# Performance work log

Measured on AMD Instinct MI355X. Metric: run time of the kernel, lower is better.

Reference implementation:

```python
import jax, jax.numpy as jnp
import numpy as np

B, L, D_MODEL, D_K, HEADS, C = 4, 4096, 512, 64, 8, 2
TOPK = int(C * np.log(L))  # int(c * log(input_seq_len)) = 16


def setup_inputs() -> dict:
    key = jax.random.key(0)
    ks = jax.random.split(key, 5)
    q_in = jax.random.normal(ks[0], (B, L, D_MODEL), jnp.float32)
    k_in = jax.random.normal(ks[1], (B, L, D_MODEL), jnp.float32)
    v_in = jax.random.normal(ks[2], (B, L, D_MODEL), jnp.float32)
    Wq = jax.random.normal(ks[3], (D_MODEL, D_K), jnp.float32) / np.sqrt(D_MODEL)
    bq = jax.random.normal(ks[4], (D_K,), jnp.float32) * 0.01
    return {"q_in": q_in, "k_in": k_in, "v_in": v_in, "Wq": Wq, "bq": bq}


def _to_heads(x, Wq, bq):
    # Faithful to original: ALL of q/k/v use the `query` Dense layer, and all
    # heads are identical copies (same projection stacked `heads` times).
    p = x @ Wq + bq                       # [B, L, d_k]
    p = jnp.swapaxes(p, 1, 2)             # [B, d_k, L]  (transpose [0,3,2,1] of [B,L,d,H])
    return jnp.broadcast_to(p[:, None], (p.shape[0], HEADS, D_K, p.shape[-1]))  # [B,H,d,L]


def reference(q_in, k_in, v_in, Wq, bq):
    Q = jnp.fft.fft(_to_heads(q_in, Wq, bq).astype(jnp.complex64), axis=-1)
    K = jnp.fft.fft(_to_heads(k_in, Wq, bq).astype(jnp.complex64), axis=-1)
    V = _to_heads(v_in, Wq, bq)           # [B,H,d,L] float32
    QK = jnp.fft.ifft(Q * jnp.conj(K), axis=-1)   # circular cross-correlation
    qk_abs = jnp.abs(QK)                  # [B,H,d,L]

    vals, idx = jax.lax.top_k(qk_abs, TOPK)       # [B,H,d,k]
    w = jax.nn.softmax(vals, axis=-1)             # softmax over the k lags

    # tf.roll(v, shift=-lag): out[t] = v[(t + lag) mod L]  -> vectorized gather
    t = jnp.arange(L, dtype=jnp.int32)
    gidx = (idx[..., None] + t) % L               # [B,H,d,k,L]
    Vk = jnp.broadcast_to(V[:, :, :, None, :], gidx.shape)
    rolled = jnp.take_along_axis(Vk, gidx, axis=-1)           # [B,H,d,k,L]
    agg = jnp.sum(rolled * w[..., None], axis=3)              # [B,H,d,L]

    out = agg.reshape(agg.shape[0], HEADS * D_K, L)           # [B, H*d, L]
    return jnp.transpose(out, (0, 2, 1))                      # [B, L, H*d]
```

## Files before the change

kernel.cpp:

```cpp
#include <hip/hip_runtime.h>
#include <hip/hip_bf16.h>

#define BQ 4
#define LQ 4096
#define DM 512
#define DK 64
#define NROWS (BQ * DK)
#define TOPK 16
#define CAND 32

typedef __attribute__((ext_vector_type(8))) short short8v;
typedef __attribute__((ext_vector_type(16))) float f32x16;

__device__ __forceinline__ unsigned short f2bf(float x) {
  unsigned u = __builtin_bit_cast(unsigned, x);
  return (unsigned short)((u + 0x7FFFu + ((u >> 16) & 1u)) >> 16);
}
__device__ __forceinline__ float bf2f(unsigned short h) {
  unsigned u = ((unsigned)h) << 16;
  return __builtin_bit_cast(float, u);
}

__device__ __forceinline__ void mfma_drain() {
  __builtin_amdgcn_sched_barrier(0);
  asm volatile("s_nop 7\n\ts_nop 7\n\ts_nop 7\n\ts_nop 7" ::: "memory");
  __builtin_amdgcn_sched_barrier(0);
}

__global__ __launch_bounds__(256) void wprep_kernel(
    const float* __restrict__ Wq, short* __restrict__ wpack) {
  const int ks = blockIdx.x;
  const int t = threadIdx.x;
  const int lane = t & 63, half = t >> 6;
  const int plane = half >> 1, nt = half & 1;
  const int r = nt * 32 + (lane & 31);
  const int kb = 16 * ks + 8 * (lane >> 5);
  short8v o;
#pragma unroll
  for (int i = 0; i < 8; ++i) {
    float v = Wq[(size_t)(kb + i) * DK + r];
    unsigned short h = f2bf(v);
    o[i] = plane ? (short)f2bf(v - bf2f(h)) : (short)h;
  }
  *(short8v*)(&wpack[(((size_t)plane * 2 + nt) * 32 + ks) * 512 + lane * 8]) = o;
}

__global__ __launch_bounds__(256) void proj_kernel(
    const float* __restrict__ q_in, const float* __restrict__ k_in,
    const float* __restrict__ v_in, const short* __restrict__ wpack,
    const float* __restrict__ bq, float* __restrict__ ws) {
  const float* x = blockIdx.z == 0 ? q_in : (blockIdx.z == 1 ? k_in : v_in);
  float* outp = ws + (size_t)blockIdx.z * (size_t)(NROWS * LQ);

  __shared__ __align__(16) float ts[8 * 1088];

  const int tid = threadIdx.x;
  const int l = tid & 63, wv = tid >> 6;
  const int gw = blockIdx.x * 4 + wv;
  const int R0 = gw * 32;
  const int koff = 8 * (l >> 5);

  const float* xb = x + (size_t)(R0 + (l & 31)) * DM + koff;
  const short* wp0 = wpack + l * 8;

  f32x16 acc[2];
#pragma unroll
  for (int nt = 0; nt < 2; ++nt)
#pragma unroll
    for (int i = 0; i < 16; ++i) acc[nt][i] = 0.f;

  float4 a0[8], a1[8];
#pragma unroll
  for (int s = 0; s < 4; ++s) {
    a0[2 * s]     = *(const float4*)(xb + s * 16);
    a0[2 * s + 1] = *(const float4*)(xb + s * 16 + 4);
  }

  short8v wc[4], wn[4];
#define WLOAD(dst, ksg)                                                      \
  do {                                                                       \
    dst[0] = *(const short8v*)(wp0 + (((ksg) + 0) << 9));                    \
    dst[1] = *(const short8v*)(wp0 + (((ksg) + 64) << 9));                   \
    dst[2] = *(const short8v*)(wp0 + (((ksg) + 32) << 9));                   \
    dst[3] = *(const short8v*)(wp0 + (((ksg) + 96) << 9));                   \
  } while (0)
  WLOAD(wc, 0);

#pragma unroll
  for (int kb = 0; kb < 8; ++kb) {
    if (kb < 7) {
#pragma unroll
      for (int s = 0; s < 4; ++s) {
        a1[2 * s]     = *(const float4*)(xb + (kb + 1) * 64 + s * 16);
        a1[2 * s + 1] = *(const float4*)(xb + (kb + 1) * 64 + s * 16 + 4);
      }
    }
#pragma unroll
    for (int s = 0; s < 4; ++s) {
      const int ksg = kb * 4 + s;
      if (ksg < 31) WLOAD(wn, ksg + 1);
      float f[8] = {a0[2 * s].x, a0[2 * s].y, a0[2 * s].z, a0[2 * s].w,
                    a0[2 * s + 1].x, a0[2 * s + 1].y, a0[2 * s + 1].z,
                    a0[2 * s + 1].w};
      short8v ah, al;
#pragma unroll
      for (int i = 0; i < 8; ++i) {
        unsigned short h = f2bf(f[i]);
        ah[i] = (short)h;
        al[i] = (short)f2bf(f[i] - bf2f(h));
      }
      asm volatile(
          "s_nop 4\n\t"
          "v_mfma_f32_32x32x16_bf16 %0, %2, %4, %0\n\t"
          "v_mfma_f32_32x32x16_bf16 %0, %2, %5, %0\n\t"
          "v_mfma_f32_32x32x16_bf16 %0, %3, %4, %0\n\t"
          "v_mfma_f32_32x32x16_bf16 %1, %2, %6, %1\n\t"
          "v_mfma_f32_32x32x16_bf16 %1, %2, %7, %1\n\t"
          "v_mfma_f32_32x32x16_bf16 %1, %3, %6, %1\n\t"
          "s_nop 7\n\t"
          "s_nop 3"
          : "+v"(acc[0]), "+v"(acc[1])
          : "v"(ah), "v"(al), "v"(wc[0]), "v"(wc[1]), "v"(wc[2]), "v"(wc[3]));
      if (ksg < 31) {
#pragma unroll
        for (int i = 0; i < 4; ++i) wc[i] = wn[i];
      }
    }
    if (kb < 7) {
#pragma unroll
      for (int i = 0; i < 8; ++i) a0[i] = a1[i];
    }
  }
#undef WLOAD

  mfma_drain();
  const int b = R0 >> 12, i0 = R0 & (LQ - 1);
  float bb[2] = {bq[l & 31], bq[32 + (l & 31)]};
#pragma unroll
  for (int nt = 0; nt < 2; ++nt) {
    float* area = ts + (wv * 2 + nt) * 1088;
#pragma unroll
    for (int r = 0; r < 16; ++r) {
      int io = (r & 3) + 8 * (r >> 2) + 4 * (l >> 5);
      area[(l & 31) * 34 + io] = acc[nt][r] + bb[nt];
    }
  }
  __syncthreads();
  const int e = l & 15, jg = l >> 4;
#pragma unroll
  for (int nt = 0; nt < 2; ++nt) {
    const float* area = ts + (wv * 2 + nt) * 1088;
#pragma unroll
    for (int p = 0; p < 8; ++p) {
      int jj = jg * 8 + p;
      float2 v = *reinterpret_cast<const float2*>(area + jj * 34 + e * 2);
      *reinterpret_cast<float2*>(
          &outp[((size_t)b * DK + nt * 32 + jj) * LQ + i0 + e * 2]) = v;
    }
  }
}

__global__ __launch_bounds__(512) void corr_topk_kernel(
    const float* __restrict__ qp, const float* __restrict__ kp,
    float* __restrict__ lw) {
  const int row = blockIdx.x;
  const int tid = threadIdx.x;
  __shared__ __align__(16) short qs[3 * 4112 + 4096];
  __shared__ __align__(16) short ks[4096];
  __shared__ __align__(16) float qf[LQ];
  __shared__ __align__(16) float kf[LQ];
  __shared__ unsigned wk[128];
  __shared__ unsigned scand[CAND];
  __shared__ float rS[CAND];
  __shared__ float ordv[TOPK]; __shared__ int ordl[TOPK];

  const float* qr = qp + ((size_t)row << 12);
  const float* kr = kp + ((size_t)row << 12);

  {
    const float4* q4 = (const float4*)qr;
    float4 v0 = q4[tid * 2], v1 = q4[tid * 2 + 1];
    float4 v2 = q4[(tid * 2 + 2) & 1023];
    ((float4*)qf)[tid * 2] = v0;
    ((float4*)qf)[tid * 2 + 1] = v1;
    float f[12] = {v0.x, v0.y, v0.z, v0.w, v1.x, v1.y, v1.z, v1.w,
                   v2.x, v2.y, v2.z, v2.w};
#pragma unroll
    for (int r = 0; r < 4; ++r) {
      short8v o;
#pragma unroll
      for (int i = 0; i < 8; ++i) o[i] = (short)f2bf(f[i + r]);
      *(short8v*)(&qs[r * 4112 + tid * 8]) = o;
    }
    const float4* k4 = (const float4*)kr;
    float4 w0 = k4[tid * 2], w1 = k4[tid * 2 + 1];
    ((float4*)kf)[tid * 2] = w0;
    ((float4*)kf)[tid * 2 + 1] = w1;
    float g[8] = {w0.x, w0.y, w0.z, w0.w, w1.x, w1.y, w1.z, w1.w};
    int Q = tid;
    int Qs = Q ^ ((Q >> 3) & 7);
    short8v o;
#pragma unroll
    for (int i = 0; i < 8; ++i) o[i] = (short)f2bf(g[i]);
    *(short8v*)(&ks[Qs << 3]) = o;
  }
  __syncthreads();

  const int l = tid & 63, wv = tid >> 6;
  const int Oq = ((8 * (l >> 5) - 32 * (l & 31)) & 4095) >> 3;
  const int rB = (l & 31) & 3;
  const int Ce = (l & 31) + 8 * (l >> 5) - rB;
  const short* qb = qs + rB * 4112;

  f32x16 acc[4];
#pragma unroll
  for (int M = 0; M < 4; ++M)
#pragma unroll
    for (int i = 0; i < 16; ++i) acc[M][i] = 0.f;

  const int J0 = wv * 32;
#pragma unroll 2
  for (int jb = 0; jb < 32; ++jb) {
    const int J = J0 + jb;
    int e1 = (Ce + 16 * J) & 4095;
    int e2 = (e1 + 4) & 4095;
    uint2 blo = *(const uint2*)(qb + e1);
    uint2 bhi = *(const uint2*)(qb + e2);
    int4 bi; bi.x = blo.x; bi.y = blo.y; bi.z = bhi.x; bi.w = bhi.y;
    short8v bf = __builtin_bit_cast(short8v, bi);
    const int Dq = 2 * J;
#pragma unroll
    for (int M = 0; M < 4; ++M) {
      int Q = (Oq + Dq - 128 * M) & 511;
      Q ^= (Q >> 3) & 7;
      short8v af = *(const short8v*)(&ks[Q << 3]);
      asm volatile("s_nop 4\n\t"
                   "v_mfma_f32_32x32x16_bf16 %0, %1, %2, %0\n\t"
                   "s_nop 7\n\t"
                   "s_nop 3"
                   : "+v"(acc[M]) : "v"(af), "v"(bf));
    }
  }

  mfma_drain();
  __syncthreads();
  float* red = (float*)qs;
  const int strip = (wv & 1) * 4096;
  const int ch4 = (l >> 5) * 4, cn = l & 31;
#define RIDX(M, r) (strip + ((M) << 10) + 32 * (((r)&3) + 8 * ((r) >> 2) + ch4) + cn)
  if (wv < 2) {
#pragma unroll
    for (int M = 0; M < 4; ++M)
#pragma unroll
      for (int r = 0; r < 16; ++r) red[RIDX(M, r)] = acc[M][r];
  }
  __syncthreads();
  if (wv >= 2 && wv < 4) {
#pragma unroll
    for (int M = 0; M < 4; ++M)
#pragma unroll
      for (int r = 0; r < 16; ++r) red[RIDX(M, r)] += acc[M][r];
  }
  __syncthreads();
  if (wv >= 4 && wv < 6) {
#pragma unroll
    for (int M = 0; M < 4; ++M)
#pragma unroll
      for (int r = 0; r < 16; ++r) red[RIDX(M, r)] += acc[M][r];
  }
  __syncthreads();
  if (wv >= 6) {
#pragma unroll
    for (int M = 0; M < 4; ++M)
#pragma unroll
      for (int r = 0; r < 16; ++r) red[RIDX(M, r)] += acc[M][r];
  }
  __syncthreads();
#undef RIDX

  {
    unsigned key[8];
#pragma unroll
    for (int i = 0; i < 8; ++i) {
      int tau = wv * 512 + i * 64 + l;
      float v = red[tau] + red[4096 + tau];
      unsigned u = __builtin_bit_cast(unsigned, fabsf(v));
      key[i] = (u & 0xFFFFF000u) | (unsigned)(4095 - tau);
    }
    unsigned bkey = key[0];
#pragma unroll
    for (int i = 1; i < 8; ++i) bkey = key[i] > bkey ? key[i] : bkey;
    for (int round = 0; round < 16; ++round) {
      unsigned m = bkey;
#pragma unroll
      for (int off = 1; off < 64; off <<= 1) {
        unsigned o = __shfl_xor(m, off);
        m = o > m ? o : m;
      }
      if (l == 0) wk[wv * 16 + round] = m;
#pragma unroll
      for (int i = 0; i < 8; ++i) key[i] = (key[i] == m) ? 0u : key[i];
      bkey = key[0];
#pragma unroll
      for (int i = 1; i < 8; ++i) bkey = key[i] > bkey ? key[i] : bkey;
    }
  }
  __syncthreads();

  if (tid < 128) {
    unsigned ki = wk[tid];
    int rank = 0;
    for (int j = 0; j < 128; ++j) rank += (wk[j] > ki);
    if (rank < CAND) scand[rank] = ki;
  }
  __syncthreads();

  {
    const int ci = tid >> 4, sub = tid & 15;
    const int lag = 4095 - (int)(scand[ci] & 0xFFFu);
    float S0 = 0.f, S1 = 0.f, S2 = 0.f, S3 = 0.f;
    for (int it = 0; it < 256; it += 4) {
      int t0 = (it + 0) * 16 + sub, t1 = (it + 1) * 16 + sub;
      int t2 = (it + 2) * 16 + sub, t3 = (it + 3) * 16 + sub;
      S0 = fmaf(kf[t0], qf[(t0 + lag) & 4095], S0);
      S1 = fmaf(kf[t1], qf[(t1 + lag) & 4095], S1);
      S2 = fmaf(kf[t2], qf[(t2 + lag) & 4095], S2);
      S3 = fmaf(kf[t3], qf[(t3 + lag) & 4095], S3);
    }
    float S = (S0 + S1) + (S2 + S3);
    S += __shfl_xor(S, 1);
    S += __shfl_xor(S, 2);
    S += __shfl_xor(S, 4);
    S += __shfl_xor(S, 8);
    if (sub == 0) rS[ci] = S;
  }
  __syncthreads();

  if (tid < CAND) {
    float vi = fabsf(rS[tid]);
    int ii = 4095 - (int)(scand[tid] & 0xFFFu);
    int rank = 0;
    for (int j = 0; j < CAND; ++j) {
      float vj = fabsf(rS[j]);
      int ij = 4095 - (int)(scand[j] & 0xFFFu);
      rank += (vj > vi) || (vj == vi && ij < ii);
    }
    if (rank < TOPK) { ordv[rank] = vi; ordl[rank] = ii; }
  }
  __syncthreads();

  if (tid == 0) {
    float m0 = ordv[0], s = 0.f, e[TOPK];
    for (int k = 0; k < TOPK; ++k) { e[k] = expf(ordv[k] - m0); s += e[k]; }
    float inv = 1.f / s;
    int* ip = (int*)(lw + (size_t)row * 32);
    for (int k = 0; k < TOPK; ++k) {
      ip[k] = ordl[k];
      ((float*)ip)[TOPK + k] = e[k] * inv;
    }
  }
}

__global__ void agg_kernel(const float* __restrict__ vpT,
                           const float* __restrict__ lw,
                           float* __restrict__ aggT) {
  const int row = blockIdx.x, tid = threadIdx.x;
  __shared__ __align__(16) float vr[2 * LQ];
  __shared__ float w[TOPK]; __shared__ int lg[TOPK];

  const float* v0 = vpT + (size_t)row * LQ;
  for (int x = tid; x < LQ; x += 256) {
    float val = v0[x];
    vr[x] = val; vr[x + LQ] = val;
  }
  if (tid < TOPK) {
    lg[tid] = ((const int*)(lw + (size_t)row * 32))[tid];
    w[tid] = lw[(size_t)row * 32 + TOPK + tid];
  }
  __syncthreads();

  float wr[TOPK]; int lr[TOPK];
#pragma unroll
  for (int k = 0; k < TOPK; ++k) { wr[k] = w[k]; lr[k] = lg[k]; }

  for (int m = 0; m < 16; ++m) {
    int t = m * 256 + tid;
    float a = 0.f;
#pragma unroll
    for (int k = 0; k < TOPK; ++k) a = fmaf(wr[k], vr[t + lr[k]], a);
    aggT[(size_t)row * LQ + t] = a;
  }
}

__global__ void trans_kernel(const float* __restrict__ aggT,
                             float* __restrict__ out) {
  const int b = blockIdx.y;
  const int t0 = blockIdx.x * 64;
  const int tid = threadIdx.x;
  __shared__ float ts[64][65];

#pragma unroll
  for (int v = 0; v < 16; ++v) {
    int f = v * 256 + tid;
    int d = f >> 6, tt = f & 63;
    ts[d][tt] = aggT[((size_t)b * DK + d) * LQ + t0 + tt];
  }
  __syncthreads();

#pragma unroll
  for (int v = 0; v < 128; ++v) {
    int f = v * 256 + tid;
    int tt = f >> 9, c = f & 511;
    out[((size_t)b * LQ + t0 + tt) * (8 * DK) + c] = ts[c & 63][tt];
  }
}

extern "C" void kernel_launch(void* const* d_in, const int* in_sizes, int n_in,
                              void* d_out, int out_size, void* d_ws, size_t ws_size,
                              hipStream_t stream) {
  const float* q_in = (const float*)d_in[0];
  const float* k_in = (const float*)d_in[1];
  const float* v_in = (const float*)d_in[2];
  const float* Wq   = (const float*)d_in[3];
  const float* bq   = (const float*)d_in[4];
  float* out = (float*)d_out;
  float* ws  = (float*)d_ws;

  const size_t M = (size_t)NROWS * LQ;
  float* qp    = ws;
  float* kp    = ws + M;
  float* vp    = ws + 2 * M;
  float* lw    = ws + 3 * M;
  float* aggT  = ws + 4 * M;
  short* wpack = (short*)(ws + 5 * M);

  wprep_kernel<<<32, 256, 0, stream>>>(Wq, wpack);
  proj_kernel<<<dim3(128, 1, 3), 256, 0, stream>>>(q_in, k_in, v_in, wpack,
                                                   bq, ws);
  corr_topk_kernel<<<NROWS, 512, 0, stream>>>(qp, kp, lw);
  agg_kernel<<<NROWS, 256, 0, stream>>>(vp, lw, aggT);
  trans_kernel<<<dim3(LQ / 64, BQ), 256, 0, stream>>>(aggT, out);
}
```

Baseline: 80.72 us.

## Split projection K dimension across wave pairs with LDS reduction

```diff
diff --git a/kernel.cpp b/kernel.cpp
--- a/kernel.cpp
+++ b/kernel.cpp
@@ -52,15 +52,15 @@
   const float* x = blockIdx.z == 0 ? q_in : (blockIdx.z == 1 ? k_in : v_in);
   float* outp = ws + (size_t)blockIdx.z * (size_t)(NROWS * LQ);
 
-  __shared__ __align__(16) float ts[8 * 1088];
+  __shared__ __align__(16) float smem[4352];
 
   const int tid = threadIdx.x;
   const int l = tid & 63, wv = tid >> 6;
-  const int gw = blockIdx.x * 4 + wv;
-  const int R0 = gw * 32;
+  const int tile = wv >> 1, kh = wv & 1;
+  const int R0 = blockIdx.x * 64 + tile * 32;
   const int koff = 8 * (l >> 5);
 
-  const float* xb = x + (size_t)(R0 + (l & 31)) * DM + koff;
+  const float* xb = x + (size_t)(R0 + (l & 31)) * DM + kh * 256 + koff;
   const short* wp0 = wpack + l * 8;
 
   f32x16 acc[2];
@@ -77,18 +77,19 @@
   }
 
   short8v wc[4], wn[4];
-#define WLOAD(dst, ksg)                                                      \
+#define WLOAD(dst, ksl)                                                      \
   do {                                                                       \
-    dst[0] = *(const short8v*)(wp0 + (((ksg) + 0) << 9));                    \
-    dst[1] = *(const short8v*)(wp0 + (((ksg) + 64) << 9));                   \
-    dst[2] = *(const short8v*)(wp0 + (((ksg) + 32) << 9));                   \
-    dst[3] = *(const short8v*)(wp0 + (((ksg) + 96) << 9));                   \
+    const int kg = kh * 16 + (ksl);                                          \
+    dst[0] = *(const short8v*)(wp0 + ((kg + 0) << 9));                       \
+    dst[1] = *(const short8v*)(wp0 + ((kg + 64) << 9));                      \
+    dst[2] = *(const short8v*)(wp0 + ((kg + 32) << 9));                      \
+    dst[3] = *(const short8v*)(wp0 + ((kg + 96) << 9));                      \
   } while (0)
   WLOAD(wc, 0);
 
 #pragma unroll
-  for (int kb = 0; kb < 8; ++kb) {
-    if (kb < 7) {
+  for (int kb = 0; kb < 4; ++kb) {
+    if (kb < 3) {
 #pragma unroll
       for (int s = 0; s < 4; ++s) {
         a1[2 * s]     = *(const float4*)(xb + (kb + 1) * 64 + s * 16);
@@ -97,8 +98,8 @@
     }
 #pragma unroll
     for (int s = 0; s < 4; ++s) {
-      const int ksg = kb * 4 + s;
-      if (ksg < 31) WLOAD(wn, ksg + 1);
+      const int ksl = kb * 4 + s;
+      if (ksl < 15) WLOAD(wn, ksl + 1);
       float f[8] = {a0[2 * s].x, a0[2 * s].y, a0[2 * s].z, a0[2 * s].w,
                     a0[2 * s + 1].x, a0[2 * s + 1].y, a0[2 * s + 1].z,
                     a0[2 * s + 1].w};
@@ -121,12 +122,12 @@
           "s_nop 3"
           : "+v"(acc[0]), "+v"(acc[1])
           : "v"(ah), "v"(al), "v"(wc[0]), "v"(wc[1]), "v"(wc[2]), "v"(wc[3]));
-      if (ksg < 31) {
+      if (ksl < 15) {
 #pragma unroll
         for (int i = 0; i < 4; ++i) wc[i] = wn[i];
       }
     }
-    if (kb < 7) {
+    if (kb < 3) {
 #pragma unroll
       for (int i = 0; i < 8; ++i) a0[i] = a1[i];
     }
@@ -134,28 +135,42 @@
 #undef WLOAD
 
   mfma_drain();
-  const int b = R0 >> 12, i0 = R0 & (LQ - 1);
-  float bb[2] = {bq[l & 31], bq[32 + (l & 31)]};
-#pragma unroll
-  for (int nt = 0; nt < 2; ++nt) {
-    float* area = ts + (wv * 2 + nt) * 1088;
-#pragma unroll
-    for (int r = 0; r < 16; ++r) {
-      int io = (r & 3) + 8 * (r >> 2) + 4 * (l >> 5);
-      area[(l & 31) * 34 + io] = acc[nt][r] + bb[nt];
-    }
-  }
-  __syncthreads();
-  const int e = l & 15, jg = l >> 4;
-#pragma unroll
-  for (int nt = 0; nt < 2; ++nt) {
-    const float* area = ts + (wv * 2 + nt) * 1088;
-#pragma unroll
-    for (int p = 0; p < 8; ++p) {
-      int jj = jg * 8 + p;
-      float2 v = *reinterpret_cast<const float2*>(area + jj * 34 + e * 2);
-      *reinterpret_cast<float2*>(
-          &outp[((size_t)b * DK + nt * 32 + jj) * LQ + i0 + e * 2]) = v;
+  if (kh == 1) {
+#pragma unroll
+    for (int nt = 0; nt < 2; ++nt)
+#pragma unroll
+      for (int r = 0; r < 16; ++r)
+        smem[tile * 2048 + nt * 1024 + r * 64 + l] = acc[nt][r];
+  }
+  __syncthreads();
+  if (kh == 0) {
+#pragma unroll
+    for (int nt = 0; nt < 2; ++nt)
+#pragma unroll
+      for (int r = 0; r < 16; ++r)
+        acc[nt][r] += smem[tile * 2048 + nt * 1024 + r * 64 + l];
+  }
+  __syncthreads();
+
+  if (kh == 0) {
+    const int b = R0 >> 12, i0 = R0 & (LQ - 1);
+    float bb[2] = {bq[l & 31], bq[32 + (l & 31)]};
+#pragma unroll
+    for (int nt = 0; nt < 2; ++nt) {
+      float* area = smem + (tile * 2 + nt) * 1088;
+#pragma unroll
+      for (int r = 0; r < 16; ++r) {
+        int io = (r & 3) + 8 * (r >> 2) + 4 * (l >> 5);
+        area[(l & 31) * 34 + io] = acc[nt][r] + bb[nt];
+      }
+      const int e = l & 15, jg = l >> 4;
+#pragma unroll
+      for (int p = 0; p < 8; ++p) {
+        int jj = jg * 8 + p;
+        float2 v = *reinterpret_cast<const float2*>(area + jj * 34 + e * 2);
+        *reinterpret_cast<float2*>(
+            &outp[((size_t)b * DK + nt * 32 + jj) * LQ + i0 + e * 2]) = v;
+      }
     }
   }
 }
@@ -435,7 +450,7 @@
   short* wpack = (short*)(ws + 5 * M);
 
   wprep_kernel<<<32, 256, 0, stream>>>(Wq, wpack);
-  proj_kernel<<<dim3(128, 1, 3), 256, 0, stream>>>(q_in, k_in, v_in, wpack,
+  proj_kernel<<<dim3(256, 1, 3), 256, 0, stream>>>(q_in, k_in, v_in, wpack,
                                                    bq, ws);
   corr_topk_kernel<<<NROWS, 512, 0, stream>>>(qp, kp, lw);
   agg_kernel<<<NROWS, 256, 0, stream>>>(vp, lw, aggT);
```

Measured after the change: 76.15 us. 1.06x faster.

## Split projection K-dimension across waves with LDS staging and cross-wave reduction

Applied to the files above, without the earlier changes.

```diff
diff --git a/kernel.cpp b/kernel.cpp
--- a/kernel.cpp
+++ b/kernel.cpp
@@ -9,6 +9,7 @@
 #define TOPK 16
 #define CAND 32
 
+typedef __attribute__((ext_vector_type(4))) float f32x4;
 typedef __attribute__((ext_vector_type(8))) short short8v;
 typedef __attribute__((ext_vector_type(16))) float f32x16;
 
@@ -19,6 +20,12 @@
 __device__ __forceinline__ float bf2f(unsigned short h) {
   unsigned u = ((unsigned)h) << 16;
   return __builtin_bit_cast(float, u);
+}
+
+__device__ __forceinline__ void gl_lds16(const float* g, float* s) {
+  auto g1 = (const __attribute__((address_space(1))) float*)(uintptr_t)g;
+  auto s3 = (__attribute__((address_space(3))) float*)(uint32_t)(uintptr_t)s;
+  __builtin_amdgcn_global_load_lds(g1, s3, 16, 0, 0);
 }
 
 __device__ __forceinline__ void mfma_drain() {
@@ -26,6 +33,12 @@
   asm volatile("s_nop 7\n\ts_nop 7\n\ts_nop 7\n\ts_nop 7" ::: "memory");
   __builtin_amdgcn_sched_barrier(0);
 }
+
+#define VMCNT(n)                                            \
+  do {                                                      \
+    asm volatile("s_waitcnt vmcnt(" #n ")" ::: "memory");   \
+    __builtin_amdgcn_sched_barrier(0);                      \
+  } while (0)
 
 __global__ __launch_bounds__(256) void wprep_kernel(
     const float* __restrict__ Wq, short* __restrict__ wpack) {
@@ -45,23 +58,45 @@
   *(short8v*)(&wpack[(((size_t)plane * 2 + nt) * 32 + ks) * 512 + lane * 8]) = o;
 }
 
-__global__ __launch_bounds__(256) void proj_kernel(
+#define WLOADR(buf, ksg_)                                                      \
+  do {                                                                         \
+    const short* wb_ = wp0 + ((size_t)(ksg_) << 9);                            \
+    asm volatile("global_load_dwordx4 %0, %1, off" : "=v"(buf[0]) : "v"(wb_)); \
+    asm volatile("global_load_dwordx4 %0, %1, off" : "=v"(buf[1]) : "v"(wb_ + (64 << 9))); \
+    asm volatile("global_load_dwordx4 %0, %1, off" : "=v"(buf[2]) : "v"(wb_ + (32 << 9))); \
+    asm volatile("global_load_dwordx4 %0, %1, off" : "=v"(buf[3]) : "v"(wb_ + (96 << 9))); \
+  } while (0)
+
+__global__ __launch_bounds__(256, 2) void proj_kernel(
     const float* __restrict__ q_in, const float* __restrict__ k_in,
     const float* __restrict__ v_in, const short* __restrict__ wpack,
     const float* __restrict__ bq, float* __restrict__ ws) {
   const float* x = blockIdx.z == 0 ? q_in : (blockIdx.z == 1 ? k_in : v_in);
   float* outp = ws + (size_t)blockIdx.z * (size_t)(NROWS * LQ);
 
-  __shared__ __align__(16) float ts[8 * 1088];
+  __shared__ __align__(16) float xs[16384];
 
   const int tid = threadIdx.x;
   const int l = tid & 63, wv = tid >> 6;
-  const int gw = blockIdx.x * 4 + wv;
-  const int R0 = gw * 32;
-  const int koff = 8 * (l >> 5);
-
-  const float* xb = x + (size_t)(R0 + (l & 31)) * DM + koff;
+  const int r = l & 31, hi = l >> 5;
+  const int R0 = blockIdx.x * 32;
+
+  float* slice = xs + wv * 4096;
+
+  {
+    const float* xw = x + (size_t)R0 * DM + 128 * wv;
+#pragma unroll
+    for (int j = 0; j < 16; ++j) {
+      const int row = 2 * j + hi;
+      const float* src = xw + (size_t)row * DM + ((r ^ (row & 7)) << 2);
+      gl_lds16(src, slice + j * 256);
+    }
+  }
+
   const short* wp0 = wpack + l * 8;
+  short8v wr3[3][4];
+  WLOADR(wr3[0], 8 * wv + 0);
+  WLOADR(wr3[1], 8 * wv + 1);
 
   f32x16 acc[2];
 #pragma unroll
@@ -69,87 +104,70 @@
 #pragma unroll
     for (int i = 0; i < 16; ++i) acc[nt][i] = 0.f;
 
-  float4 a0[8], a1[8];
-#pragma unroll
-  for (int s = 0; s < 4; ++s) {
-    a0[2 * s]     = *(const float4*)(xb + s * 16);
-    a0[2 * s + 1] = *(const float4*)(xb + s * 16 + 4);
-  }
-
-  short8v wc[4], wn[4];
-#define WLOAD(dst, ksg)                                                      \
-  do {                                                                       \
-    dst[0] = *(const short8v*)(wp0 + (((ksg) + 0) << 9));                    \
-    dst[1] = *(const short8v*)(wp0 + (((ksg) + 64) << 9));                   \
-    dst[2] = *(const short8v*)(wp0 + (((ksg) + 32) << 9));                   \
-    dst[3] = *(const short8v*)(wp0 + (((ksg) + 96) << 9));                   \
-  } while (0)
-  WLOAD(wc, 0);
-
-#pragma unroll
-  for (int kb = 0; kb < 8; ++kb) {
-    if (kb < 7) {
-#pragma unroll
-      for (int s = 0; s < 4; ++s) {
-        a1[2 * s]     = *(const float4*)(xb + (kb + 1) * 64 + s * 16);
-        a1[2 * s + 1] = *(const float4*)(xb + (kb + 1) * 64 + s * 16 + 4);
-      }
-    }
-#pragma unroll
-    for (int s = 0; s < 4; ++s) {
-      const int ksg = kb * 4 + s;
-      if (ksg < 31) WLOAD(wn, ksg + 1);
-      float f[8] = {a0[2 * s].x, a0[2 * s].y, a0[2 * s].z, a0[2 * s].w,
-                    a0[2 * s + 1].x, a0[2 * s + 1].y, a0[2 * s + 1].z,
-                    a0[2 * s + 1].w};
-      short8v ah, al;
-#pragma unroll
-      for (int i = 0; i < 8; ++i) {
-        unsigned short h = f2bf(f[i]);
-        ah[i] = (short)h;
-        al[i] = (short)f2bf(f[i] - bf2f(h));
-      }
-      asm volatile(
-          "s_nop 4\n\t"
-          "v_mfma_f32_32x32x16_bf16 %0, %2, %4, %0\n\t"
-          "v_mfma_f32_32x32x16_bf16 %0, %2, %5, %0\n\t"
-          "v_mfma_f32_32x32x16_bf16 %0, %3, %4, %0\n\t"
-          "v_mfma_f32_32x32x16_bf16 %1, %2, %6, %1\n\t"
-          "v_mfma_f32_32x32x16_bf16 %1, %2, %7, %1\n\t"
-          "v_mfma_f32_32x32x16_bf16 %1, %3, %6, %1\n\t"
-          "s_nop 7\n\t"
-          "s_nop 3"
-          : "+v"(acc[0]), "+v"(acc[1])
-          : "v"(ah), "v"(al), "v"(wc[0]), "v"(wc[1]), "v"(wc[2]), "v"(wc[3]));
-      if (ksg < 31) {
-#pragma unroll
-        for (int i = 0; i < 4; ++i) wc[i] = wn[i];
-      }
-    }
-    if (kb < 7) {
-#pragma unroll
-      for (int i = 0; i < 8; ++i) a0[i] = a1[i];
-    }
-  }
-#undef WLOAD
+  const float* rbase = slice + r * 128;
+  const int c = r & 7;
+
+#pragma unroll
+  for (int kl = 0; kl < 8; ++kl) {
+    if (kl < 6) WLOADR(wr3[(kl + 2) % 3], 8 * wv + kl + 2);
+    if (kl < 6) VMCNT(8);
+    else if (kl == 6) VMCNT(4);
+    else VMCNT(0);
+
+    const int q0 = 4 * kl + 2 * hi;
+    f32x4 xa = *(const f32x4*)(rbase + ((q0 ^ c) << 2));
+    f32x4 xb2 = *(const f32x4*)(rbase + (((q0 + 1) ^ c) << 2));
+    float f[8] = {xa[0], xa[1], xa[2], xa[3], xb2[0], xb2[1], xb2[2], xb2[3]};
+    short8v ah, al;
+#pragma unroll
+    for (int i = 0; i < 8; ++i) {
+      unsigned short h = f2bf(f[i]);
+      ah[i] = (short)h;
+      al[i] = (short)f2bf(f[i] - bf2f(h));
+    }
+    short8v* w_ = wr3[kl % 3];
+    asm volatile(
+        "s_nop 4\n\t"
+        "v_mfma_f32_32x32x16_bf16 %0, %2, %4, %0\n\t"
+        "v_mfma_f32_32x32x16_bf16 %0, %2, %5, %0\n\t"
+        "v_mfma_f32_32x32x16_bf16 %0, %3, %4, %0\n\t"
+        "v_mfma_f32_32x32x16_bf16 %1, %2, %6, %1\n\t"
+        "v_mfma_f32_32x32x16_bf16 %1, %2, %7, %1\n\t"
+        "v_mfma_f32_32x32x16_bf16 %1, %3, %6, %1\n\t"
+        "s_nop 7\n\t"
+        "s_nop 3"
+        : "+v"(acc[0]), "+v"(acc[1])
+        : "v"(ah), "v"(al), "v"(w_[0]), "v"(w_[1]), "v"(w_[2]), "v"(w_[3]));
+  }
 
   mfma_drain();
-  const int b = R0 >> 12, i0 = R0 & (LQ - 1);
-  float bb[2] = {bq[l & 31], bq[32 + (l & 31)]};
-#pragma unroll
-  for (int nt = 0; nt < 2; ++nt) {
-    float* area = ts + (wv * 2 + nt) * 1088;
-#pragma unroll
-    for (int r = 0; r < 16; ++r) {
-      int io = (r & 3) + 8 * (r >> 2) + 4 * (l >> 5);
-      area[(l & 31) * 34 + io] = acc[nt][r] + bb[nt];
-    }
-  }
-  __syncthreads();
-  const int e = l & 15, jg = l >> 4;
-#pragma unroll
-  for (int nt = 0; nt < 2; ++nt) {
-    const float* area = ts + (wv * 2 + nt) * 1088;
+#pragma unroll
+  for (int nt = 0; nt < 2; ++nt)
+#pragma unroll
+    for (int rr = 0; rr < 16; ++rr)
+      slice[nt * 1024 + rr * 64 + l] = acc[nt][rr];
+  __syncthreads();
+
+  if (wv < 2) {
+    const int nt = wv;
+    float sacc[16];
+#pragma unroll
+    for (int rr = 0; rr < 16; ++rr)
+      sacc[rr] = xs[0 * 4096 + nt * 1024 + rr * 64 + l] +
+                 xs[1 * 4096 + nt * 1024 + rr * 64 + l] +
+                 xs[2 * 4096 + nt * 1024 + rr * 64 + l] +
+                 xs[3 * 4096 + nt * 1024 + rr * 64 + l];
+    float* area = xs + wv * 4096 + 2048;
+    const float bb = bq[nt * 32 + r];
+#pragma unroll
+    for (int rr = 0; rr < 16; ++rr) {
+      int io = (rr & 3) + 8 * (rr >> 2) + 4 * hi;
+      area[r * 34 + io] = sacc[rr] + bb;
+    }
+    asm volatile("s_waitcnt lgkmcnt(0)" ::: "memory");
+    __builtin_amdgcn_sched_barrier(0);
+    const int e = l & 15, jg = l >> 4;
+    const int b = R0 >> 12, i0 = R0 & (LQ - 1);
 #pragma unroll
     for (int p = 0; p < 8; ++p) {
       int jj = jg * 8 + p;
@@ -234,10 +252,7 @@
       int Q = (Oq + Dq - 128 * M) & 511;
       Q ^= (Q >> 3) & 7;
       short8v af = *(const short8v*)(&ks[Q << 3]);
-      asm volatile("s_nop 4\n\t"
-                   "v_mfma_f32_32x32x16_bf16 %0, %1, %2, %0\n\t"
-                   "s_nop 7\n\t"
-                   "s_nop 3"
+      asm volatile("v_mfma_f32_32x32x16_bf16 %0, %1, %2, %0"
                    : "+v"(acc[M]) : "v"(af), "v"(bf));
     }
   }
@@ -435,7 +450,7 @@
   short* wpack = (short*)(ws + 5 * M);
 
   wprep_kernel<<<32, 256, 0, stream>>>(Wq, wpack);
-  proj_kernel<<<dim3(128, 1, 3), 256, 0, stream>>>(q_in, k_in, v_in, wpack,
+  proj_kernel<<<dim3(512, 1, 3), 256, 0, stream>>>(q_in, k_in, v_in, wpack,
                                                    bq, ws);
   corr_topk_kernel<<<NROWS, 512, 0, stream>>>(qp, kp, lw);
   agg_kernel<<<NROWS, 256, 0, stream>>>(vp, lw, aggT);
```

Result: faster. 77.34 us (-4.2%).
